# Optimization experiments

Hardware: AMD Instinct MI355X
Metric: run time of the kernel (lower is better)

Reference implementation:

```python
import jax, jax.numpy as jnp
import numpy as np

# Config: B=4, S=2048, E=512, H=8 heads, D=E//H=64, FF=2048.
# QLayer (quantum circuit) is replaced by its linear stand-in matching the
# declared I/O dims: V: D->D per head, Q/K: D->1 (scalar per token).

EPS = 1e-5

def layernorm(x):
    # torch LayerNorm(elementwise_affine=False), population variance
    mu = jnp.mean(x, axis=-1, keepdims=True)
    var = jnp.var(x, axis=-1, keepdims=True)
    return (x - mu) / jnp.sqrt(var + EPS)


def setup_inputs() -> dict:
    key = jax.random.key(0)
    ks = jax.random.split(key, 12)
    B, S, E, H = 4, 2048, 512, 8
    D = E // H
    F = 2048
    u = lambda k, shape, fan: jax.random.uniform(k, shape, jnp.float32, -1.0 / np.sqrt(fan), 1.0 / np.sqrt(fan))
    return {
        "input1": jax.random.normal(ks[0], (B, S, E), jnp.float32),
        # per-head value projection D->D
        "Wv": u(ks[1], (H, D, D), D),
        "bv": u(ks[2], (H, D), D),
        # per-head scalar query / key projections D->1
        "Wq": u(ks[3], (H, D), D),
        "bq": u(ks[4], (H,), D),
        "Wk": u(ks[5], (H, D), D),
        "bk": u(ks[6], (H,), D),
        # merger MLP: E->F (GELU) -> E
        "W1": u(ks[7], (E, F), E),
        "b1": u(ks[8], (F,), E),
        "W2": u(ks[9], (F, E), F),
        "b2": u(ks[10], (E,), F),
    }


def reference(input1, Wv, bv, Wq, bq, Wk, bk, W1, b1, W2, b2):
    B, S, E = input1.shape
    H, D, _ = Wv.shape
    x = layernorm(input1)
    # chunk along last dim == reshape into heads
    xh = x.reshape(B, S, H, D)
    # per-head projections (vectorized over heads)
    V = jnp.einsum('bshd,hde->bshe', xh, Wv) + bv            # [B,S,H,D]
    Q = jnp.einsum('bshd,hd->bhs', xh, Wq) + bq[None, :, None]  # [B,H,S]
    K = jnp.einsum('bshd,hd->bhs', xh, Wk) + bk[None, :, None]  # [B,H,S]
    # quadratic-distance scores: A = -(Q - K)^2, [B,H,S,S]
    A = -jnp.square(Q[:, :, :, None] - K[:, :, None, :])
    attn = jax.nn.softmax(A * (1.0 / np.sqrt(D)), axis=-1)
    head_out = jnp.einsum('bhqk,bkhd->bqhd', attn, V).reshape(B, S, E)
    # merger: Linear -> GELU (exact) -> Linear, plus residual
    h = jax.nn.gelu(head_out @ W1 + b1, approximate=False)
    return h @ W2 + b2 + input1
```

## Files before the change

### kernel.cpp

```cpp
#include <hip/hip_runtime.h>
#include <hip/hip_bf16.h>


#define Bsz 4
#define Ssz 2048
#define Esz 512
#define Hsz 8
#define Dsz 64
#define Fsz 2048
#define NR 16

typedef __attribute__((ext_vector_type(8))) short bf16x8;
typedef __attribute__((ext_vector_type(4))) float f32x4;

__device__ __constant__ float RS[16] = {
    0.f, 1.0f, 0.70710678f, 0.57735027f, 0.5f, 0.44721360f, 0.40824829f,
    0.37796447f, 0.35355339f, 0.33333333f, 0.31622777f, 0.30151134f,
    0.28867513f, 0.27735010f, 0.26726124f, 0.25819889f};

static __device__ __forceinline__ void gload_lds16(const void* g, void* l) {
    __builtin_amdgcn_global_load_lds(
        (const __attribute__((address_space(1))) unsigned int*)g,
        (__attribute__((address_space(3))) unsigned int*)l, 16, 0, 0);
}

__global__ __launch_bounds__(256) void ln_qkv_kernel(
    const float* __restrict__ x,
    const float* __restrict__ Wv, const float* __restrict__ bv,
    const float* __restrict__ Wq, const float* __restrict__ bq,
    const float* __restrict__ Wk, const float* __restrict__ bk,
    float* __restrict__ Qo, float* __restrict__ Ko, float* __restrict__ Vo)
{
    int tok = blockIdx.x;
    int b = tok >> 11, s = tok & 2047;
    int t = threadIdx.x;

    __shared__ float xn[512];
    __shared__ float red[256];

    const float* xrow = x + (size_t)tok * Esz;
    float x0 = xrow[t], x1 = xrow[t + 256];

    red[t] = x0 + x1;
    __syncthreads();
    for (int o = 128; o > 0; o >>= 1) { if (t < o) red[t] += red[t + o]; __syncthreads(); }
    float mean = red[0] * (1.0f / 512.0f);
    __syncthreads();
    float d0 = x0 - mean, d1 = x1 - mean;
    red[t] = d0 * d0 + d1 * d1;
    __syncthreads();
    for (int o = 128; o > 0; o >>= 1) { if (t < o) red[t] += red[t + o]; __syncthreads(); }
    float inv = rsqrtf(red[0] * (1.0f / 512.0f) + 1e-5f);

    xn[t] = d0 * inv;
    xn[t + 256] = d1 * inv;
    __syncthreads();

    #pragma unroll
    for (int rep = 0; rep < 2; ++rep) {
        int o = t + rep * 256;
        int h = o >> 6, dd = o & 63;
        const float* w = Wv + (size_t)(h * 64) * 64 + dd;
        const float* xh = xn + h * 64;
        float acc = bv[o];
        #pragma unroll
        for (int e = 0; e < 64; ++e) acc = fmaf(xh[e], w[(size_t)e * 64], acc);
        Vo[((size_t)(b * Hsz + h) * Ssz + s) * Dsz + dd] = acc;
    }

    if (t < 16) {
        int h = t & 7;
        const float* w = (t < 8 ? Wq : Wk) + h * 64;
        const float* xh = xn + h * 64;
        float acc = 0.0f;
        #pragma unroll
        for (int e = 0; e < 64; ++e) acc = fmaf(xh[e], w[e], acc);
        acc += (t < 8 ? bq[h] : bk[h]);
        float* outp = (t < 8 ? Qo : Ko);
        outp[(b * Hsz + h) * Ssz + s] = acc;
    }
}

__global__ __launch_bounds__(256) void attn_moments(
    const float* __restrict__ Kv, const float* __restrict__ Vv, float* __restrict__ Mp)
{
    int chunk = blockIdx.x, bh = blockIdx.y;
    int t = threadIdx.x;
    __shared__ float Wt[256][16];
    __shared__ float denp[4][16];

    int kg = chunk * 256 + t;
    float kv = Kv[bh * Ssz + kg];
    float wn = __expf(-0.125f * kv * kv);
    float half = 0.5f * kv;
    Wt[t][0] = wn;
    #pragma unroll
    for (int n = 1; n < NR; ++n) { wn *= half * RS[n]; Wt[t][n] = wn; }
    __syncthreads();

    int w = t >> 6, lane = t & 63;
    int ng = w * 4;
    float a0 = 0.f, a1 = 0.f, a2 = 0.f, a3 = 0.f;
    const float* vbase = Vv + ((size_t)bh * Ssz + chunk * 256) * Dsz + lane;
    for (int k = 0; k < 256; ++k) {
        float v = vbase[(size_t)k * Dsz];
        a0 = fmaf(Wt[k][ng + 0], v, a0);
        a1 = fmaf(Wt[k][ng + 1], v, a1);
        a2 = fmaf(Wt[k][ng + 2], v, a2);
        a3 = fmaf(Wt[k][ng + 3], v, a3);
    }
    size_t base = (((size_t)bh * 8 + chunk) * NR + ng) * 68 + lane;
    Mp[base + 0 * 68] = a0;
    Mp[base + 1 * 68] = a1;
    Mp[base + 2 * 68] = a2;
    Mp[base + 3 * 68] = a3;

    if (lane < 16) {
        float s = 0.f;
        for (int kk = 0; kk < 64; ++kk) s += Wt[w * 64 + kk][lane];
        denp[w][lane] = s;
    }
    __syncthreads();
    if (t < 16) {
        float m = denp[0][t] + denp[1][t] + denp[2][t] + denp[3][t];
        Mp[(((size_t)bh * 8 + chunk) * NR + t) * 68 + 64] = m;
    }
}

__global__ __launch_bounds__(256) void attn_reduce(
    const float* __restrict__ Mp, float* __restrict__ M)
{
    int bh = blockIdx.x, t = threadIdx.x;
    for (int i = t; i < NR * 68; i += 256) {
        float s = 0.f;
        #pragma unroll
        for (int c = 0; c < 8; ++c)
            s += Mp[(((size_t)bh * 8 + c) * NR) * 68 + i];
        M[(size_t)bh * NR * 68 + i] = s;
    }
}

__global__ __launch_bounds__(256) void attn_apply(
    const float* __restrict__ Qv, const float* __restrict__ M, __hip_bfloat16* __restrict__ A1)
{
    int tok = blockIdx.x;
    int b = tok >> 11, s = tok & 2047;
    int t = threadIdx.x;
    #pragma unroll
    for (int rep = 0; rep < 2; ++rep) {
        int e = t + rep * 256;
        int h = e >> 6, d = e & 63;
        int bh = b * 8 + h;
        float q = Qv[bh * Ssz + s];
        const float* Mb = M + (size_t)bh * NR * 68;
        float half = 0.5f * q;
        float phi = 1.0f;
        float num = Mb[d], den = Mb[64];
        #pragma unroll
        for (int n = 1; n < NR; ++n) {
            phi *= half * RS[n];
            num = fmaf(phi, Mb[n * 68 + d], num);
            den = fmaf(phi, Mb[n * 68 + 64], den);
        }
        A1[(size_t)tok * Esz + e] = __float2bfloat16(num / den);
    }
}

__global__ __launch_bounds__(256) void transpose_bf16(
    const float* __restrict__ in, __hip_bfloat16* __restrict__ out, int R, int C)
{
    __shared__ float tile[32][33];
    int bx = blockIdx.x, by = blockIdx.y;
    int t = threadIdx.x;
    int tc = t & 31, tr = t >> 5;
    #pragma unroll
    for (int i = 0; i < 4; ++i) {
        int r = by * 32 + tr + i * 8, c = bx * 32 + tc;
        tile[tr + i * 8][tc] = in[(size_t)r * C + c];
    }
    __syncthreads();
    #pragma unroll
    for (int i = 0; i < 4; ++i) {
        int ro = bx * 32 + tr + i * 8, co = by * 32 + tc;
        out[(size_t)ro * R + co] = __float2bfloat16(tile[tc][tr + i * 8]);
    }
}

template <int KDIM, int EPI>
__global__ __launch_bounds__(256) void gemm_bf16(
    const __hip_bfloat16* __restrict__ A, const __hip_bfloat16* __restrict__ Bt,
    const float* __restrict__ bias, const float* __restrict__ resid,
    void* __restrict__ Out, int N)
{
    __shared__ unsigned short As[128][32];
    __shared__ unsigned short Bs[128][32];
    int t = threadIdx.x;
    int w = t >> 6, lane = t & 63;
    int wr = w >> 1, wc = w & 1;
    int bm = blockIdx.y * 128, bn = blockIdx.x * 128;

    f32x4 acc[4][4] = {};
    const int r = t >> 2, cg = (t & 3) * 8;

    for (int k0 = 0; k0 < KDIM; k0 += 32) {
        gload_lds16(&A[(size_t)(bm + r) * KDIM + k0 + cg], &As[r][cg]);
        gload_lds16(&A[(size_t)(bm + r + 64) * KDIM + k0 + cg], &As[r + 64][cg]);
        gload_lds16(&Bt[(size_t)(bn + r) * KDIM + k0 + cg], &Bs[r][cg]);
        gload_lds16(&Bt[(size_t)(bn + r + 64) * KDIM + k0 + cg], &Bs[r + 64][cg]);
        __syncthreads();
        bf16x8 af[4], bfr[4];
        #pragma unroll
        for (int i = 0; i < 4; ++i) {
            af[i]  = *(const bf16x8*)&As[wr * 64 + i * 16 + (lane & 15)][(lane >> 4) * 8];
            bfr[i] = *(const bf16x8*)&Bs[wc * 64 + i * 16 + (lane & 15)][(lane >> 4) * 8];
        }
        #pragma unroll
        for (int i = 0; i < 4; ++i)
            #pragma unroll
            for (int j = 0; j < 4; ++j)
                acc[i][j] = __builtin_amdgcn_mfma_f32_16x16x32_bf16(af[i], bfr[j], acc[i][j], 0, 0, 0);
        __syncthreads();
    }

    int col0 = lane & 15, rowg = lane >> 4;
    #pragma unroll
    for (int i = 0; i < 4; ++i) {
        #pragma unroll
        for (int j = 0; j < 4; ++j) {
            #pragma unroll
            for (int v = 0; v < 4; ++v) {
                int m = bm + wr * 64 + i * 16 + rowg * 4 + v;
                int n = bn + wc * 64 + j * 16 + col0;
                float val = acc[i][j][v] + bias[n];
                if (EPI == 0) {
                    float g = 0.5f * val * (1.0f + erff(val * 0.70710678f));
                    ((__hip_bfloat16*)Out)[(size_t)m * N + n] = __float2bfloat16(g);
                } else {
                    size_t idx = (size_t)m * N + n;
                    ((float*)Out)[idx] = val + resid[idx];
                }
            }
        }
    }
}

extern "C" void kernel_launch(void* const* d_in, const int* in_sizes, int n_in,
                              void* d_out, int out_size, void* d_ws, size_t ws_size,
                              hipStream_t stream) {
    const float* x  = (const float*)d_in[0];
    const float* Wv = (const float*)d_in[1];
    const float* bv = (const float*)d_in[2];
    const float* Wq = (const float*)d_in[3];
    const float* bq = (const float*)d_in[4];
    const float* Wk = (const float*)d_in[5];
    const float* bk = (const float*)d_in[6];
    const float* W1 = (const float*)d_in[7];
    const float* b1 = (const float*)d_in[8];
    const float* W2 = (const float*)d_in[9];
    const float* b2 = (const float*)d_in[10];
    float* out = (float*)d_out;

    char* ws = (char*)d_ws;
    float* Qb    = (float*)(ws + 0);
    float* Kb    = (float*)(ws + 262144);
    float* Vb    = (float*)(ws + 524288);
    float* Mpart = (float*)(ws + 17301504);
    float* Mfull = (float*)(ws + 18415616);
    __hip_bfloat16* A1   = (__hip_bfloat16*)(ws + 18554880);
    __hip_bfloat16* W1T  = (__hip_bfloat16*)(ws + 26943488);
    __hip_bfloat16* W2T  = (__hip_bfloat16*)(ws + 29040640);
    __hip_bfloat16* hbuf = (__hip_bfloat16*)(ws + 31137792);

    ln_qkv_kernel<<<dim3(Bsz * Ssz), 256, 0, stream>>>(x, Wv, bv, Wq, bq, Wk, bk, Qb, Kb, Vb);
    attn_moments<<<dim3(8, Bsz * Hsz), 256, 0, stream>>>(Kb, Vb, Mpart);
    attn_reduce<<<dim3(Bsz * Hsz), 256, 0, stream>>>(Mpart, Mfull);
    attn_apply<<<dim3(Bsz * Ssz), 256, 0, stream>>>(Qb, Mfull, A1);
    transpose_bf16<<<dim3(Fsz / 32, Esz / 32), 256, 0, stream>>>(W1, W1T, Esz, Fsz);
    transpose_bf16<<<dim3(Esz / 32, Fsz / 32), 256, 0, stream>>>(W2, W2T, Fsz, Esz);
    gemm_bf16<Esz, 0><<<dim3(Fsz / 128, (Bsz * Ssz) / 128), 256, 0, stream>>>(A1, W1T, b1, nullptr, hbuf, Fsz);
    gemm_bf16<Fsz, 1><<<dim3(Esz / 128, (Bsz * Ssz) / 128), 256, 0, stream>>>(hbuf, W2T, b2, x, out, Esz);
}
```

Before: 243.2 us.

## Defer V projection into moment transform and warp-per-token layernorm

Because V is linear in the normalized input, the moments are now accumulated over normalized x (stored in bf16) and the per-head Wv/bv projection is applied once to the small moment matrices instead of to every token. This removes the per-token 64x64 matvec and the fp32 V buffer write and read. The layernorm kernel now processes one token per wavefront with shuffle reductions in place of LDS tree reductions, and moment chunks are halved to 128 keys for more blocks. The bf16 storage of normalized x adds rounding error to the moments.

Result: faster. 210.1 us (-13.6%).

```diff
diff --git a/kernel.cpp b/kernel.cpp
--- a/kernel.cpp
+++ b/kernel.cpp
@@ -9,6 +9,8 @@
 #define Dsz 64
 #define Fsz 2048
 #define NR 16
+#define NCH 16
+#define CHK 128
 
 typedef __attribute__((ext_vector_type(8))) short bf16x8;
 typedef __attribute__((ext_vector_type(4))) float f32x4;
@@ -24,119 +26,144 @@
         (__attribute__((address_space(3))) unsigned int*)l, 16, 0, 0);
 }
 
-__global__ __launch_bounds__(256) void ln_qkv_kernel(
+static __device__ __forceinline__ unsigned short f2bf(float f) {
+    unsigned int b = __float_as_uint(f);
+    b += 0x7FFFu + ((b >> 16) & 1u);
+    return (unsigned short)(b >> 16);
+}
+
+__global__ __launch_bounds__(256) void ln_qk_kernel(
     const float* __restrict__ x,
-    const float* __restrict__ Wv, const float* __restrict__ bv,
     const float* __restrict__ Wq, const float* __restrict__ bq,
     const float* __restrict__ Wk, const float* __restrict__ bk,
-    float* __restrict__ Qo, float* __restrict__ Ko, float* __restrict__ Vo)
-{
-    int tok = blockIdx.x;
+    float* __restrict__ Qo, float* __restrict__ Ko, __hip_bfloat16* __restrict__ Xn)
+{
+    int wid = threadIdx.x >> 6, lane = threadIdx.x & 63;
+    int tok = blockIdx.x * 4 + wid;
     int b = tok >> 11, s = tok & 2047;
-    int t = threadIdx.x;
-
-    __shared__ float xn[512];
-    __shared__ float red[256];
 
     const float* xrow = x + (size_t)tok * Esz;
-    float x0 = xrow[t], x1 = xrow[t + 256];
-
-    red[t] = x0 + x1;
-    __syncthreads();
-    for (int o = 128; o > 0; o >>= 1) { if (t < o) red[t] += red[t + o]; __syncthreads(); }
-    float mean = red[0] * (1.0f / 512.0f);
-    __syncthreads();
-    float d0 = x0 - mean, d1 = x1 - mean;
-    red[t] = d0 * d0 + d1 * d1;
-    __syncthreads();
-    for (int o = 128; o > 0; o >>= 1) { if (t < o) red[t] += red[t + o]; __syncthreads(); }
-    float inv = rsqrtf(red[0] * (1.0f / 512.0f) + 1e-5f);
-
-    xn[t] = d0 * inv;
-    xn[t + 256] = d1 * inv;
-    __syncthreads();
-
-    #pragma unroll
-    for (int rep = 0; rep < 2; ++rep) {
-        int o = t + rep * 256;
-        int h = o >> 6, dd = o & 63;
-        const float* w = Wv + (size_t)(h * 64) * 64 + dd;
-        const float* xh = xn + h * 64;
-        float acc = bv[o];
-        #pragma unroll
-        for (int e = 0; e < 64; ++e) acc = fmaf(xh[e], w[(size_t)e * 64], acc);
-        Vo[((size_t)(b * Hsz + h) * Ssz + s) * Dsz + dd] = acc;
-    }
-
-    if (t < 16) {
-        int h = t & 7;
-        const float* w = (t < 8 ? Wq : Wk) + h * 64;
-        const float* xh = xn + h * 64;
-        float acc = 0.0f;
-        #pragma unroll
-        for (int e = 0; e < 64; ++e) acc = fmaf(xh[e], w[e], acc);
-        acc += (t < 8 ? bq[h] : bk[h]);
-        float* outp = (t < 8 ? Qo : Ko);
-        outp[(b * Hsz + h) * Ssz + s] = acc;
+    float4 v0 = *(const float4*)&xrow[lane * 8];
+    float4 v1 = *(const float4*)&xrow[lane * 8 + 4];
+
+    float sum = v0.x + v0.y + v0.z + v0.w + v1.x + v1.y + v1.z + v1.w;
+    #pragma unroll
+    for (int off = 32; off > 0; off >>= 1) sum += __shfl_xor(sum, off);
+    float mean = sum * (1.0f / 512.0f);
+
+    float d[8] = {v0.x - mean, v0.y - mean, v0.z - mean, v0.w - mean,
+                  v1.x - mean, v1.y - mean, v1.z - mean, v1.w - mean};
+    float ss = 0.f;
+    #pragma unroll
+    for (int j = 0; j < 8; ++j) ss = fmaf(d[j], d[j], ss);
+    #pragma unroll
+    for (int off = 32; off > 0; off >>= 1) ss += __shfl_xor(ss, off);
+    float inv = rsqrtf(ss * (1.0f / 512.0f) + 1e-5f);
+
+    float xn[8];
+    #pragma unroll
+    for (int j = 0; j < 8; ++j) xn[j] = d[j] * inv;
+
+    int h = lane >> 3, dsub = (lane & 7) * 8;
+    union { bf16x8 v; unsigned short u[8]; } pk;
+    #pragma unroll
+    for (int j = 0; j < 8; ++j) pk.u[j] = f2bf(xn[j]);
+    *(bf16x8*)((unsigned short*)Xn + (((size_t)(b * Hsz + h) * Ssz + s) * Dsz + dsub)) = pk.v;
+
+    float4 wqa = *(const float4*)&Wq[h * 64 + dsub];
+    float4 wqb = *(const float4*)&Wq[h * 64 + dsub + 4];
+    float4 wka = *(const float4*)&Wk[h * 64 + dsub];
+    float4 wkb = *(const float4*)&Wk[h * 64 + dsub + 4];
+    float pq = xn[0]*wqa.x + xn[1]*wqa.y + xn[2]*wqa.z + xn[3]*wqa.w
+             + xn[4]*wqb.x + xn[5]*wqb.y + xn[6]*wqb.z + xn[7]*wqb.w;
+    float pkv = xn[0]*wka.x + xn[1]*wka.y + xn[2]*wka.z + xn[3]*wka.w
+              + xn[4]*wkb.x + xn[5]*wkb.y + xn[6]*wkb.z + xn[7]*wkb.w;
+    #pragma unroll
+    for (int off = 1; off < 8; off <<= 1) {
+        pq  += __shfl_xor(pq, off);
+        pkv += __shfl_xor(pkv, off);
+    }
+    if ((lane & 7) == 0) {
+        int bh = b * Hsz + h;
+        Qo[bh * Ssz + s] = pq + bq[h];
+        Ko[bh * Ssz + s] = pkv + bk[h];
     }
 }
 
 __global__ __launch_bounds__(256) void attn_moments(
-    const float* __restrict__ Kv, const float* __restrict__ Vv, float* __restrict__ Mp)
+    const float* __restrict__ Kv, const __hip_bfloat16* __restrict__ Xn, float* __restrict__ Gp)
 {
     int chunk = blockIdx.x, bh = blockIdx.y;
     int t = threadIdx.x;
-    __shared__ float Wt[256][16];
+    __shared__ float Wt[CHK][17];
     __shared__ float denp[4][16];
 
-    int kg = chunk * 256 + t;
-    float kv = Kv[bh * Ssz + kg];
-    float wn = __expf(-0.125f * kv * kv);
-    float half = 0.5f * kv;
-    Wt[t][0] = wn;
-    #pragma unroll
-    for (int n = 1; n < NR; ++n) { wn *= half * RS[n]; Wt[t][n] = wn; }
+    if (t < CHK) {
+        float kv = Kv[bh * Ssz + chunk * CHK + t];
+        float wn = __expf(-0.125f * kv * kv);
+        float half = 0.5f * kv;
+        Wt[t][0] = wn;
+        #pragma unroll
+        for (int n = 1; n < NR; ++n) { wn *= half * RS[n]; Wt[t][n] = wn; }
+    }
     __syncthreads();
 
     int w = t >> 6, lane = t & 63;
     int ng = w * 4;
     float a0 = 0.f, a1 = 0.f, a2 = 0.f, a3 = 0.f;
-    const float* vbase = Vv + ((size_t)bh * Ssz + chunk * 256) * Dsz + lane;
-    for (int k = 0; k < 256; ++k) {
-        float v = vbase[(size_t)k * Dsz];
+    const __hip_bfloat16* xb = Xn + ((size_t)bh * Ssz + chunk * CHK) * Dsz + lane;
+    for (int k = 0; k < CHK; ++k) {
+        float v = __bfloat162float(xb[(size_t)k * Dsz]);
         a0 = fmaf(Wt[k][ng + 0], v, a0);
         a1 = fmaf(Wt[k][ng + 1], v, a1);
         a2 = fmaf(Wt[k][ng + 2], v, a2);
         a3 = fmaf(Wt[k][ng + 3], v, a3);
     }
-    size_t base = (((size_t)bh * 8 + chunk) * NR + ng) * 68 + lane;
-    Mp[base + 0 * 68] = a0;
-    Mp[base + 1 * 68] = a1;
-    Mp[base + 2 * 68] = a2;
-    Mp[base + 3 * 68] = a3;
-
-    if (lane < 16) {
+    size_t base = (((size_t)bh * NCH + chunk) * NR + ng) * 68 + lane;
+    Gp[base + 0 * 68] = a0;
+    Gp[base + 1 * 68] = a1;
+    Gp[base + 2 * 68] = a2;
+    Gp[base + 3 * 68] = a3;
+
+    if (t < 64) {
+        int n = t & 15, q = t >> 4;
         float s = 0.f;
-        for (int kk = 0; kk < 64; ++kk) s += Wt[w * 64 + kk][lane];
-        denp[w][lane] = s;
+        #pragma unroll
+        for (int kk = 0; kk < CHK / 4; ++kk) s += Wt[q * (CHK / 4) + kk][n];
+        denp[q][n] = s;
     }
     __syncthreads();
     if (t < 16) {
         float m = denp[0][t] + denp[1][t] + denp[2][t] + denp[3][t];
-        Mp[(((size_t)bh * 8 + chunk) * NR + t) * 68 + 64] = m;
-    }
-}
-
-__global__ __launch_bounds__(256) void attn_reduce(
-    const float* __restrict__ Mp, float* __restrict__ M)
-{
-    int bh = blockIdx.x, t = threadIdx.x;
+        Gp[(((size_t)bh * NCH + chunk) * NR + t) * 68 + 64] = m;
+    }
+}
+
+__global__ __launch_bounds__(256) void attn_mtransform(
+    const float* __restrict__ Gp, const float* __restrict__ Wv, const float* __restrict__ bv,
+    float* __restrict__ M)
+{
+    int bh = blockIdx.x, h = bh & 7, t = threadIdx.x;
+    __shared__ float Gf[NR * 68];
     for (int i = t; i < NR * 68; i += 256) {
         float s = 0.f;
         #pragma unroll
-        for (int c = 0; c < 8; ++c)
-            s += Mp[(((size_t)bh * 8 + c) * NR) * 68 + i];
-        M[(size_t)bh * NR * 68 + i] = s;
+        for (int c = 0; c < NCH; ++c)
+            s += Gp[(((size_t)bh * NCH + c) * NR) * 68 + i];
+        Gf[i] = s;
+    }
+    __syncthreads();
+    #pragma unroll
+    for (int rep = 0; rep < 4; ++rep) {
+        int o = t + rep * 256;
+        int n = o >> 6, dd = o & 63;
+        float den = Gf[n * 68 + 64];
+        float acc = den * bv[h * 64 + dd];
+        const float* wv = Wv + ((size_t)h * 64) * 64 + dd;
+        #pragma unroll
+        for (int e = 0; e < 64; ++e) acc = fmaf(Gf[n * 68 + e], wv[(size_t)e * 64], acc);
+        M[(size_t)bh * NR * 68 + n * 68 + dd] = acc;
+        if (dd == 0) M[(size_t)bh * NR * 68 + n * 68 + 64] = den;
     }
 }
 
@@ -149,17 +176,17 @@
     #pragma unroll
     for (int rep = 0; rep < 2; ++rep) {
         int e = t + rep * 256;
-        int h = e >> 6, d = e & 63;
+        int h = e >> 6, dd = e & 63;
         int bh = b * 8 + h;
         float q = Qv[bh * Ssz + s];
         const float* Mb = M + (size_t)bh * NR * 68;
         float half = 0.5f * q;
         float phi = 1.0f;
-        float num = Mb[d], den = Mb[64];
+        float num = Mb[dd], den = Mb[64];
         #pragma unroll
         for (int n = 1; n < NR; ++n) {
             phi *= half * RS[n];
-            num = fmaf(phi, Mb[n * 68 + d], num);
+            num = fmaf(phi, Mb[n * 68 + dd], num);
             den = fmaf(phi, Mb[n * 68 + 64], den);
         }
         A1[(size_t)tok * Esz + e] = __float2bfloat16(num / den);
@@ -263,17 +290,17 @@
     char* ws = (char*)d_ws;
     float* Qb    = (float*)(ws + 0);
     float* Kb    = (float*)(ws + 262144);
-    float* Vb    = (float*)(ws + 524288);
-    float* Mpart = (float*)(ws + 17301504);
-    float* Mfull = (float*)(ws + 18415616);
-    __hip_bfloat16* A1   = (__hip_bfloat16*)(ws + 18554880);
-    __hip_bfloat16* W1T  = (__hip_bfloat16*)(ws + 26943488);
-    __hip_bfloat16* W2T  = (__hip_bfloat16*)(ws + 29040640);
-    __hip_bfloat16* hbuf = (__hip_bfloat16*)(ws + 31137792);
-
-    ln_qkv_kernel<<<dim3(Bsz * Ssz), 256, 0, stream>>>(x, Wv, bv, Wq, bq, Wk, bk, Qb, Kb, Vb);
-    attn_moments<<<dim3(8, Bsz * Hsz), 256, 0, stream>>>(Kb, Vb, Mpart);
-    attn_reduce<<<dim3(Bsz * Hsz), 256, 0, stream>>>(Mpart, Mfull);
+    __hip_bfloat16* Xn = (__hip_bfloat16*)(ws + 524288);
+    float* Gp    = (float*)(ws + 8912896);
+    float* Mfull = (float*)(ws + 11141120);
+    __hip_bfloat16* A1   = (__hip_bfloat16*)(ws + 11280384);
+    __hip_bfloat16* W1T  = (__hip_bfloat16*)(ws + 19668992);
+    __hip_bfloat16* W2T  = (__hip_bfloat16*)(ws + 21766144);
+    __hip_bfloat16* hbuf = (__hip_bfloat16*)(ws + 23863296);
+
+    ln_qk_kernel<<<dim3((Bsz * Ssz) / 4), 256, 0, stream>>>(x, Wq, bq, Wk, bk, Qb, Kb, Xn);
+    attn_moments<<<dim3(NCH, Bsz * Hsz), 256, 0, stream>>>(Kb, Xn, Gp);
+    attn_mtransform<<<dim3(Bsz * Hsz), 256, 0, stream>>>(Gp, Wv, bv, Mfull);
     attn_apply<<<dim3(Bsz * Ssz), 256, 0, stream>>>(Qb, Mfull, A1);
     transpose_bf16<<<dim3(Fsz / 32, Esz / 32), 256, 0, stream>>>(W1, W1T, Esz, Fsz);
     transpose_bf16<<<dim3(Esz / 32, Fsz / 32), 256, 0, stream>>>(W2, W2T, Fsz, Esz);
```
